# Kernel tuning notes

Hardware: AMD Instinct MI355X
Metric: run time of the kernel (lower is better)

Reference implementation:

```python
import jax, jax.numpy as jnp
import numpy as np

NUM_SEGMENTS = 16
N_MAX = 256
CHUNK = (N_MAX + NUM_SEGMENTS - 1) // NUM_SEGMENTS  # 16
BETA1, BETA2, BETA3 = 0.5, 0.5, 0.4


def _masked_mean(x, mask):
    m = mask.astype(x.dtype)
    s = m.sum()
    return jnp.where(s > 0, (x * m).sum() / jnp.maximum(s, 1.0), jnp.zeros((), x.dtype))


def setup_inputs() -> dict:
    key = jax.random.key(0)
    ks = jax.random.split(key, 10)
    B, S, H, V, Sm, R = 2, 1024, 4096, 32000, 256, 256
    k_hidden = jax.random.normal(ks[0], (B, S, H), dtype=jnp.float32)
    last_hidden = jax.random.normal(ks[1], (B, S, H), dtype=jnp.float32)
    input_ids = jax.random.randint(ks[2], (B, S), 0, V)
    attention_mask = jnp.ones((B, S), dtype=jnp.int32)
    starts = jax.random.randint(ks[3], (B,), 0, 300)
    ends = starts + 200 + jax.random.randint(ks[4], (B,), 0, 100)
    math_lengths = jnp.full((B,), Sm, dtype=jnp.int64 if jax.config.jax_enable_x64 else jnp.int32)
    math_labels = jax.random.randint(ks[5], (B, Sm), 0, V)
    math_attention_mask = jnp.ones((B, Sm), dtype=jnp.int32)
    A_matrices = jax.random.normal(ks[6], (NUM_SEGMENTS, H, R), dtype=jnp.float32) * 0.02
    B_matrices = jax.random.normal(ks[7], (NUM_SEGMENTS, R, H), dtype=jnp.float32) * 0.02
    bias = jnp.zeros((NUM_SEGMENTS, H), dtype=jnp.float32)
    W_lm = jax.random.normal(ks[8], (H, V), dtype=jnp.float32) * 0.02
    return {"k_hidden": k_hidden, "last_hidden": last_hidden, "input_ids": input_ids,
            "attention_mask": attention_mask, "starts": starts, "ends": ends,
            "math_lengths": math_lengths, "math_labels": math_labels,
            "math_attention_mask": math_attention_mask, "A_matrices": A_matrices,
            "B_matrices": B_matrices, "bias": bias, "W_lm": W_lm}


def reference(k_hidden, last_hidden, input_ids, attention_mask, starts, ends,
              math_lengths, math_labels, math_attention_mask,
              A_matrices, B_matrices, bias, W_lm):
    B, S, H = last_hidden.shape
    Sm = math_labels.shape[1]
    n_blk = Sm // CHUNK  # == NUM_SEGMENTS here (N_max == Sm)

    # ---- simple-talk / final-answer CE losses on full logits ----
    logits = jnp.einsum('bsh,hv->bsv', last_hidden, W_lm)  # [B,S,V]
    logp = jax.nn.log_softmax(logits[:, :-1, :], axis=-1)
    labels = input_ids[:, 1:]
    nll = -jnp.take_along_axis(logp, labels[..., None], axis=-1)[..., 0]  # [B,S-1]
    idx = jnp.arange(S - 1)[None, :]
    real_len = attention_mask.sum(axis=1)[:, None]
    mask_simple = (idx >= starts[:, None] - 1) & (idx <= ends[:, None] - 1)
    mask_final = (idx >= ends[:, None]) & (idx < real_len - 1)
    simple_talk_loss = _masked_mean(nll, mask_simple)
    final_answer_loss = _masked_mean(nll, mask_final)

    # ---- math loss: segment-routed LoRA (A @ (B @ h) + bias) then lm_head CE ----
    # mask_hidden selects the contiguous block [starts, starts+math_lengths) per row;
    # with full math_attention_mask this is exactly Sm tokens per row.
    pos = starts[:, None] + jnp.arange(Sm)[None, :]  # [B,Sm]
    math_h = jnp.take_along_axis(k_hidden, pos[:, :, None], axis=1)  # [B,Sm,H]
    # segment_ids are position//CHUNK -> contiguous blocks: grouped GEMM via reshape
    hb = math_h.reshape(B, n_blk, CHUNK, H)
    inter = jnp.einsum('bsch,srh->bscr', hb, B_matrices)      # B_seg @ h
    trans = jnp.einsum('bscr,shr->bsch', inter, A_matrices)   # A_seg @ inter
    trans = trans + bias[None, :, None, :]
    t = trans.reshape(B * Sm, H)
    mlogits = t @ W_lm                                        # [B*Sm, V]
    mlogp = jax.nn.log_softmax(mlogits, axis=-1)
    tgt = math_labels.reshape(-1)
    mnll = -jnp.take_along_axis(mlogp, tgt[:, None], axis=-1)[:, 0]  # [B*Sm]
    math_loss = mnll.mean()
    # per-segment mean losses (diagnostic, no-grad in original)
    A_losses = jax.lax.stop_gradient(mnll.reshape(B, n_blk, CHUNK).mean(axis=(0, 2)))

    total_loss = BETA1 * math_loss + BETA2 * simple_talk_loss + BETA3 * final_answer_loss
    return total_loss, math_loss, simple_talk_loss, final_answer_loss, A_losses
```

## Files before the change

### kernel.cpp

```cpp
#include <hip/hip_runtime.h>

#define NSEG 16
#define CH   16
#define Bb   2
#define Ss   1024
#define Hh   4096
#define Vv   32000
#define SMm  256
#define Rr   256

#define M_MAIN 2046
#define M_MATH 512
#define M_REAL 2558
#define M_PAD  2560

#define BM 128
#define BN 128
#define BK 128
#define NT_M (M_PAD/BM)
#define NT_N (Vv/BN)
#define KT   (Hh/BK)
#define NWG  (NT_M*NT_N)
#define NQG  (Hh/16)

#define HC   8
#define HCL  (Hh/HC)
#define PART_STRIDE (Bb*NSEG*CH*Rr)

typedef __attribute__((ext_vector_type(4))) float    floatx4;
typedef __attribute__((ext_vector_type(4))) int      intx4;
typedef __attribute__((ext_vector_type(8))) int      intx8;

#define ASCALE 16.f
#define WSCALE 256.f
#define DESCALE (1.f/(16.f*256.f))

template<bool W>
__device__ __forceinline__ int cvtpk(float a, float b, int old) {
  return __builtin_amdgcn_cvt_pk_fp8_f32(a, b, old, W);
}

__device__ __forceinline__ void gload_lds16(const void* g, void* l) {
  __builtin_amdgcn_global_load_lds((const __attribute__((address_space(1))) void*)g,
                                   (__attribute__((address_space(3))) void*)l, 16, 0, 0);
}

__global__ __launch_bounds__(256) void k_convA(const float* __restrict__ lh, intx4* __restrict__ Aq) {
  int row = blockIdx.x * 256 + threadIdx.x;
  int qgg = blockIdx.y;
  if (row >= M_MAIN) return;
  int b = row / (Ss - 1), s = row % (Ss - 1);
  const floatx4* src = (const floatx4*)(lh + ((size_t)(b * Ss + s)) * Hh + qgg * 16);
  floatx4 f0 = src[0], f1 = src[1], f2 = src[2], f3 = src[3];
  int p0 = cvtpk<false>(f0[0]*ASCALE, f0[1]*ASCALE, 0); p0 = cvtpk<true>(f0[2]*ASCALE, f0[3]*ASCALE, p0);
  int p1 = cvtpk<false>(f1[0]*ASCALE, f1[1]*ASCALE, 0); p1 = cvtpk<true>(f1[2]*ASCALE, f1[3]*ASCALE, p1);
  int p2 = cvtpk<false>(f2[0]*ASCALE, f2[1]*ASCALE, 0); p2 = cvtpk<true>(f2[2]*ASCALE, f2[3]*ASCALE, p2);
  int p3 = cvtpk<false>(f3[0]*ASCALE, f3[1]*ASCALE, 0); p3 = cvtpk<true>(f3[2]*ASCALE, f3[3]*ASCALE, p3);
  Aq[(size_t)qgg * M_PAD + row] = (intx4){p0, p1, p2, p3};
}

__global__ __launch_bounds__(256) void k_convW(const float* __restrict__ W, intx4* __restrict__ Wf) {
  int v = blockIdx.x * 256 + threadIdx.x;
  int qgg = blockIdx.y;
  const float* base = W + (size_t)(qgg * 16) * Vv + v;
  int p[4];
  #pragma unroll
  for (int q = 0; q < 4; ++q) {
    float e0 = base[(size_t)(4*q+0) * Vv] * WSCALE;
    float e1 = base[(size_t)(4*q+1) * Vv] * WSCALE;
    float e2 = base[(size_t)(4*q+2) * Vv] * WSCALE;
    float e3 = base[(size_t)(4*q+3) * Vv] * WSCALE;
    int pp = cvtpk<false>(e0, e1, 0);
    p[q] = cvtpk<true>(e2, e3, pp);
  }
  Wf[(size_t)qgg * Vv + v] = (intx4){p[0], p[1], p[2], p[3]};
}

__global__ __launch_bounds__(256) void k_inter2(const float* __restrict__ kh, const float* __restrict__ Bm,
                                                const int* __restrict__ starts, float* __restrict__ part) {
  int bid = blockIdx.x;
  int b = bid >> 7, seg = (bid >> 3) & 15, hc = bid & 7;
  int tid = threadIdx.x;
  __shared__ float sX[CH][HCL];
  int st = starts[b];
  for (int i = tid; i < CH * (HCL / 4); i += 256) {
    int c = i / (HCL / 4), k4 = i % (HCL / 4);
    int pos = st + seg * CH + c;
    ((floatx4*)&sX[c][0])[k4] = *(const floatx4*)(kh + ((size_t)(b * Ss + pos)) * Hh + hc * HCL + 4 * k4);
  }
  __syncthreads();
  const floatx4* w = (const floatx4*)(Bm + ((size_t)(seg * Rr + tid)) * Hh + hc * HCL);
  float acc[CH];
  #pragma unroll
  for (int c = 0; c < CH; ++c) acc[c] = 0.f;
  for (int i = 0; i < HCL / 4; ++i) {
    floatx4 w4 = w[i];
    #pragma unroll
    for (int c = 0; c < CH; ++c)
      acc[c] += w4[0]*sX[c][4*i] + w4[1]*sX[c][4*i+1] + w4[2]*sX[c][4*i+2] + w4[3]*sX[c][4*i+3];
  }
  float* dst = part + (size_t)hc * PART_STRIDE + ((size_t)(b * NSEG + seg)) * CH * Rr;
  #pragma unroll
  for (int c = 0; c < CH; ++c) dst[c * Rr + tid] = acc[c];
}

__global__ __launch_bounds__(256) void k_trans(const float* __restrict__ part, const float* __restrict__ Am,
                                               const float* __restrict__ bias, intx4* __restrict__ Aq) {
  int bid = blockIdx.x;
  int b = bid >> 7, seg = (bid >> 3) & 15, ht = bid & 7;
  int tid = threadIdx.x;
  __shared__ float sI[CH][Rr];
  const float* ib = part + ((size_t)(b * NSEG + seg)) * CH * Rr;
  for (int i = tid; i < CH * Rr / 4; i += 256) {
    floatx4 s = ((const floatx4*)ib)[i];
    #pragma unroll
    for (int hc = 1; hc < HC; ++hc)
      s += ((const floatx4*)(ib + (size_t)hc * PART_STRIDE))[i];
    ((floatx4*)&sI[0][0])[i] = s;
  }
  __syncthreads();
  unsigned char* Ab = (unsigned char*)Aq;
  for (int hh = 0; hh < 2; ++hh) {
    int h = (ht << 9) + (tid << 1) + hh;
    const floatx4* ar = (const floatx4*)(Am + ((size_t)(seg * Hh + h)) * Rr);
    float acc[CH];
    #pragma unroll
    for (int c = 0; c < CH; ++c) acc[c] = 0.f;
    for (int i = 0; i < Rr / 4; ++i) {
      floatx4 a4 = ar[i];
      #pragma unroll
      for (int c = 0; c < CH; ++c)
        acc[c] += a4[0]*sI[c][i*4] + a4[1]*sI[c][i*4+1] + a4[2]*sI[c][i*4+2] + a4[3]*sI[c][i*4+3];
    }
    float bv = bias[seg * Hh + h];
    #pragma unroll
    for (int c = 0; c < CH; ++c) {
      int row = M_MAIN + b * SMm + seg * CH + c;
      int pk = cvtpk<false>((acc[c] + bv) * ASCALE, 0.f, 0);
      Ab[(((size_t)(h >> 4)) * M_PAD + row) * 16 + (h & 15)] = (unsigned char)(pk & 0xFF);
    }
  }
}

__global__ __launch_bounds__(256) void k_labels(const int* __restrict__ input_ids, const int* __restrict__ mlab,
                                                int* __restrict__ labels, float* __restrict__ llog,
                                                intx4* __restrict__ Aq) {
  int t = blockIdx.x * 256 + threadIdx.x;
  if (t < M_PAD) {
    int lab;
    if (t < M_MAIN)      { int b = t / (Ss - 1), s = t % (Ss - 1); lab = input_ids[b * Ss + s + 1]; }
    else if (t < M_REAL) { lab = mlab[t - M_MAIN]; }
    else                 { lab = 0x7fffffff; }
    labels[t] = lab;
    llog[t] = 0.f;
  }
  if (t < 2 * NQG) {
    int qgg = t >> 1, row = M_REAL + (t & 1);
    Aq[(size_t)qgg * M_PAD + row] = (intx4){0, 0, 0, 0};
  }
}

__global__ __launch_bounds__(256, 4) void k_gemm_mx(const intx4* __restrict__ Aq, const intx4* __restrict__ Wf,
                                                    const int* __restrict__ labels, float* __restrict__ pmax,
                                                    float* __restrict__ psum, float* __restrict__ llog) {
  __shared__ intx4 As[BK/16][BM];
  __shared__ intx4 Bs[BK/16][BN];
  __shared__ float redM[BM * 2];
  __shared__ float redS[BM * 2];

  int bid = blockIdx.x;
  int mt = bid % NT_M, nt = bid / NT_M;
  int m0 = mt * BM, n0 = nt * BN;
  int tid = threadIdx.x;
  int lane = tid & 63, wid = tid >> 6;
  int wr = wid >> 1, wc = wid & 1;
  int l15 = lane & 15, l4 = lane >> 4;

  floatx4 acc[4][4];
  #pragma unroll
  for (int m = 0; m < 4; ++m)
    #pragma unroll
    for (int n = 0; n < 4; ++n) acc[m][n] = (floatx4){0.f, 0.f, 0.f, 0.f};

  for (int kt = 0; kt < KT; ++kt) {
    __syncthreads();
    #pragma unroll
    for (int it = 0; it < 4; ++it) {
      int ci = it * 256 + tid;
      int qg = ci >> 7, row = ci & 127;
      gload_lds16((const char*)Aq + (((size_t)(kt * 8 + qg) * M_PAD + m0 + row) << 4), &As[qg][row]);
    }
    #pragma unroll
    for (int it = 0; it < 4; ++it) {
      int ci = it * 256 + tid;
      int qg = ci >> 7, col = ci & 127;
      gload_lds16((const char*)Wf + (((size_t)(kt * 8 + qg) * Vv + n0 + col) << 4), &Bs[qg][col]);
    }
    __syncthreads();

    intx8 a[4], b[4];
    #pragma unroll
    for (int m = 0; m < 4; ++m) {
      int row = m * 16 + l15;
      intx4 lo = As[2 * l4][row];
      intx4 hi = As[2 * l4 + 1][row];
      a[m] = __builtin_shufflevector(lo, hi, 0, 1, 2, 3, 4, 5, 6, 7);
    }
    #pragma unroll
    for (int n = 0; n < 4; ++n) {
      int col = wc * 64 + n * 16 + l15;
      intx4 lo = Bs[2 * l4][col];
      intx4 hi = Bs[2 * l4 + 1][col];
      b[n] = __builtin_shufflevector(lo, hi, 0, 1, 2, 3, 4, 5, 6, 7);
    }
    #pragma unroll
    for (int m = 0; m < 4; ++m)
      #pragma unroll
      for (int n = 0; n < 4; ++n)
        acc[m][n] = __builtin_amdgcn_mfma_scale_f32_16x16x128_f8f6f4(
            a[m], b[n], acc[m][n], 0, 0, 0, 0x7F7F7F7F, 0, 0x7F7F7F7F);
  }

  #pragma unroll
  for (int m = 0; m < 4; ++m)
    #pragma unroll
    for (int n = 0; n < 4; ++n) acc[m][n] *= DESCALE;

  #pragma unroll
  for (int m = 0; m < 4; ++m) {
    #pragma unroll
    for (int r = 0; r < 4; ++r) {
      int grow = m0 + wr * 64 + m * 16 + l4 * 4 + r;
      int lab = (grow < M_REAL) ? labels[grow] : -1;
      #pragma unroll
      for (int n = 0; n < 4; ++n) {
        int gcol = n0 + wc * 64 + n * 16 + l15;
        if (lab == gcol) llog[grow] = acc[m][n][r];
      }
    }
  }
  float rm[4][4];
  #pragma unroll
  for (int m = 0; m < 4; ++m)
    #pragma unroll
    for (int r = 0; r < 4; ++r) {
      float v = fmaxf(fmaxf(acc[m][0][r], acc[m][1][r]), fmaxf(acc[m][2][r], acc[m][3][r]));
      v = fmaxf(v, __shfl_xor(v, 1));
      v = fmaxf(v, __shfl_xor(v, 2));
      v = fmaxf(v, __shfl_xor(v, 4));
      v = fmaxf(v, __shfl_xor(v, 8));
      rm[m][r] = v;
    }
  if (l15 == 0) {
    #pragma unroll
    for (int m = 0; m < 4; ++m)
      #pragma unroll
      for (int r = 0; r < 4; ++r)
        redM[(wr * 64 + m * 16 + l4 * 4 + r) * 2 + wc] = rm[m][r];
  }
  __syncthreads();
  #pragma unroll
  for (int m = 0; m < 4; ++m)
    #pragma unroll
    for (int r = 0; r < 4; ++r) {
      int row = wr * 64 + m * 16 + l4 * 4 + r;
      float tmx = fmaxf(redM[row * 2], redM[row * 2 + 1]);
      float s = 0.f;
      #pragma unroll
      for (int n = 0; n < 4; ++n) s += __expf(acc[m][n][r] - tmx);
      s += __shfl_xor(s, 1);
      s += __shfl_xor(s, 2);
      s += __shfl_xor(s, 4);
      s += __shfl_xor(s, 8);
      rm[m][r] = s;
    }
  if (l15 == 0) {
    #pragma unroll
    for (int m = 0; m < 4; ++m)
      #pragma unroll
      for (int r = 0; r < 4; ++r)
        redS[(wr * 64 + m * 16 + l4 * 4 + r) * 2 + wc] = rm[m][r];
  }
  __syncthreads();
  if (tid < BM) {
    int grow = m0 + tid;
    if (grow < M_REAL) {
      float tmx = fmaxf(redM[tid * 2], redM[tid * 2 + 1]);
      float s = redS[tid * 2] + redS[tid * 2 + 1];
      pmax[(size_t)grow * NT_N + nt] = tmx;
      psum[(size_t)grow * NT_N + nt] = s;
    }
  }
}

__global__ __launch_bounds__(256) void k_fin(const float* __restrict__ pmax, const float* __restrict__ psum,
                                             const float* __restrict__ llog, float* __restrict__ nll) {
  int row = blockIdx.x * 4 + (threadIdx.x >> 6);
  int lane = threadIdx.x & 63;
  if (row >= M_REAL) return;
  float m = -3.4e38f;
  for (int t = lane; t < NT_N; t += 64) m = fmaxf(m, pmax[(size_t)row * NT_N + t]);
  #pragma unroll
  for (int d = 1; d < 64; d <<= 1) m = fmaxf(m, __shfl_xor(m, d));
  float s = 0.f;
  for (int t = lane; t < NT_N; t += 64)
    s += psum[(size_t)row * NT_N + t] * __expf(pmax[(size_t)row * NT_N + t] - m);
  #pragma unroll
  for (int d = 1; d < 64; d <<= 1) s += __shfl_xor(s, d);
  if (lane == 0) nll[row] = logf(s) + m - llog[row];
}

__global__ __launch_bounds__(256) void k_loss(const float* __restrict__ nll, const int* __restrict__ starts,
                                              const int* __restrict__ ends, const int* __restrict__ attn,
                                              float* __restrict__ out) {
  __shared__ float rA[256], rB[256], rC[256], rD[256];
  __shared__ float smath[M_MATH];
  __shared__ float rl[2];
  int tid = threadIdx.x;
  for (int b = 0; b < 2; ++b) {
    float p = 0.f;
    for (int i = tid; i < Ss; i += 256) p += (float)attn[b * Ss + i];
    rA[tid] = p;
    __syncthreads();
    if (tid == 0) { float t = 0.f; for (int i = 0; i < 256; ++i) t += rA[i]; rl[b] = t; }
    __syncthreads();
  }
  float ss = 0.f, sc = 0.f, fs = 0.f, fc = 0.f;
  int st0 = starts[0], st1 = starts[1], en0 = ends[0], en1 = ends[1];
  for (int r = tid; r < M_MAIN; r += 256) {
    int b = r / (Ss - 1), idx = r % (Ss - 1);
    int st = b ? st1 : st0, en = b ? en1 : en0;
    int rlen = (int)rl[b];
    float v = nll[r];
    if (idx >= st - 1 && idx <= en - 1) { ss += v; sc += 1.f; }
    if (idx >= en && idx < rlen - 1)    { fs += v; fc += 1.f; }
  }
  rA[tid] = ss; rB[tid] = sc; rC[tid] = fs; rD[tid] = fc;
  for (int j = tid; j < M_MATH; j += 256) smath[j] = nll[M_MAIN + j];
  __syncthreads();
  if (tid == 0) {
    float SS = 0.f, SC = 0.f, FS = 0.f, FC = 0.f;
    for (int i = 0; i < 256; ++i) { SS += rA[i]; SC += rB[i]; FS += rC[i]; FC += rD[i]; }
    float MS = 0.f;
    for (int j = 0; j < M_MATH; ++j) MS += smath[j];
    float math_loss = MS / (float)M_MATH;
    float simple = (SC > 0.f) ? SS / fmaxf(SC, 1.f) : 0.f;
    float fin    = (FC > 0.f) ? FS / fmaxf(FC, 1.f) : 0.f;
    out[0] = 0.5f * math_loss + 0.5f * simple + 0.4f * fin;
    out[1] = math_loss;
    out[2] = simple;
    out[3] = fin;
    for (int seg = 0; seg < NSEG; ++seg) {
      float a = 0.f;
      for (int b = 0; b < 2; ++b)
        for (int c = 0; c < CH; ++c) a += smath[b * SMm + seg * CH + c];
      out[4 + seg] = a / 32.f;
    }
  }
}

extern "C" void kernel_launch(void* const* d_in, const int* in_sizes, int n_in,
                              void* d_out, int out_size, void* d_ws, size_t ws_size,
                              hipStream_t stream) {
  const float* k_hidden    = (const float*)d_in[0];
  const float* last_hidden = (const float*)d_in[1];
  const int*   input_ids   = (const int*)d_in[2];
  const int*   attn        = (const int*)d_in[3];
  const int*   starts      = (const int*)d_in[4];
  const int*   ends        = (const int*)d_in[5];
  const int*   math_labels = (const int*)d_in[7];
  const float* A_matrices  = (const float*)d_in[9];
  const float* B_matrices  = (const float*)d_in[10];
  const float* bias        = (const float*)d_in[11];
  const float* W_lm        = (const float*)d_in[12];
  float* out = (float*)d_out;

  char* ws = (char*)d_ws;
  size_t off = 0;
  intx4* Wf   = (intx4*)ws;                 off += (size_t)NQG * Vv * 16;
  intx4* Aq   = (intx4*)(ws + off);         off += (size_t)NQG * M_PAD * 16;
  float* part = (float*)(ws + off);         off += (size_t)HC * PART_STRIDE * 4;
  int*   labels = (int*)(ws + off);         off += (size_t)M_PAD * 4;
  float* llog   = (float*)(ws + off);       off += (size_t)M_PAD * 4;
  float* pmax   = (float*)(ws + off);       off += (size_t)M_PAD * NT_N * 4;
  float* psum   = (float*)(ws + off);       off += (size_t)M_PAD * NT_N * 4;
  float* nll    = (float*)(ws + off);       off += (size_t)M_PAD * 4;

  {
    dim3 ga((M_MAIN + 255) / 256, NQG);
    k_convA<<<ga, 256, 0, stream>>>(last_hidden, Aq);
  }
  k_inter2<<<Bb * NSEG * HC, 256, 0, stream>>>(k_hidden, B_matrices, starts, part);
  k_trans<<<Bb * NSEG * 8, 256, 0, stream>>>(part, A_matrices, bias, Aq);
  k_labels<<<(M_PAD + 255) / 256, 256, 0, stream>>>(input_ids, math_labels, labels, llog, Aq);
  {
    dim3 gw(Vv / 256, NQG);
    k_convW<<<gw, 256, 0, stream>>>(W_lm, Wf);
  }
  k_gemm_mx<<<NWG, 256, 0, stream>>>(Aq, Wf, labels, pmax, psum, llog);
  k_fin<<<(M_REAL + 3) / 4, 256, 0, stream>>>(pmax, psum, llog, nll);
  k_loss<<<1, 256, 0, stream>>>(nll, starts, ends, attn, out);
}
```

Before: 625.0 us.

## Enlarge GEMM tile to 256 rows and add triple-buffered async LDS pipeline

The FP8 MX GEMM now uses 512-thread workgroups with a 256x128 tile, so each W tile is reused across twice as many rows and the number of workgroups is halved. Global-to-LDS loads become a three-stage ring buffer issued two K-steps ahead, with vmcnt waits and a single barrier per iteration in place of the two syncthreads. Priority is raised around the MFMA block. This costs more LDS per block and lower occupancy, and the epilogue reduction must now handle the larger BM, which the hidden code may or may not do correctly.

```diff
diff --git a/kernel.cpp b/kernel.cpp
--- a/kernel.cpp
+++ b/kernel.cpp
@@ -14,7 +14,7 @@
 #define M_REAL 2558
 #define M_PAD  2560
 
-#define BM 128
+#define BM 256
 #define BN 128
 #define BK 128
 #define NT_M (M_PAD/BM)
@@ -160,11 +160,11 @@
   }
 }
 
-__global__ __launch_bounds__(256, 4) void k_gemm_mx(const intx4* __restrict__ Aq, const intx4* __restrict__ Wf,
-                                                    const int* __restrict__ labels, float* __restrict__ pmax,
-                                                    float* __restrict__ psum, float* __restrict__ llog) {
-  __shared__ intx4 As[BK/16][BM];
-  __shared__ intx4 Bs[BK/16][BN];
+__global__ __launch_bounds__(512, 2) void k_gemm_mx2(const intx4* __restrict__ Aq, const intx4* __restrict__ Wf,
+                                                     const int* __restrict__ labels, float* __restrict__ pmax,
+                                                     float* __restrict__ psum, float* __restrict__ llog) {
+  __shared__ intx4 As[3][8][BM];
+  __shared__ intx4 Bs[3][8][BN];
   __shared__ float redM[BM * 2];
   __shared__ float redS[BM * 2];
 
@@ -172,7 +172,8 @@
   int mt = bid % NT_M, nt = bid / NT_M;
   int m0 = mt * BM, n0 = nt * BN;
   int tid = threadIdx.x;
-  int lane = tid & 63, wid = tid >> 6;
+  int lane = tid & 63;
+  int wid = tid >> 6;
   int wr = wid >> 1, wc = wid & 1;
   int l15 = lane & 15, l4 = lane >> 4;
 
@@ -182,49 +183,73 @@
     #pragma unroll
     for (int n = 0; n < 4; ++n) acc[m][n] = (floatx4){0.f, 0.f, 0.f, 0.f};
 
+#define STAGE(tt, bb) do {                                                              \
+    const intx4* ab_ = Aq + (size_t)(tt) * 8 * M_PAD;                                   \
+    _Pragma("unroll")                                                                   \
+    for (int it_ = 0; it_ < 4; ++it_) {                                                 \
+      int s_ = it_ * 512 + tid;                                                         \
+      gload_lds16(ab_ + ((size_t)(s_ >> 8) * M_PAD + m0 + (s_ & 255)),                  \
+                  (void*)(&As[bb][0][0] + s_));                                         \
+    }                                                                                   \
+    const intx4* wb_ = Wf + (size_t)(tt) * 8 * Vv;                                      \
+    _Pragma("unroll")                                                                   \
+    for (int it_ = 0; it_ < 2; ++it_) {                                                 \
+      int s_ = it_ * 512 + tid;                                                         \
+      gload_lds16(wb_ + ((size_t)(s_ >> 7) * Vv + n0 + (s_ & 127)),                     \
+                  (void*)(&Bs[bb][0][0] + s_));                                         \
+    }                                                                                   \
+  } while (0)
+
+  STAGE(0, 0);
+  STAGE(1, 1);
+  int cur = 0;
+
   for (int kt = 0; kt < KT; ++kt) {
-    __syncthreads();
-    #pragma unroll
-    for (int it = 0; it < 4; ++it) {
-      int ci = it * 256 + tid;
-      int qg = ci >> 7, row = ci & 127;
-      gload_lds16((const char*)Aq + (((size_t)(kt * 8 + qg) * M_PAD + m0 + row) << 4), &As[qg][row]);
-    }
-    #pragma unroll
-    for (int it = 0; it < 4; ++it) {
-      int ci = it * 256 + tid;
-      int qg = ci >> 7, col = ci & 127;
-      gload_lds16((const char*)Wf + (((size_t)(kt * 8 + qg) * Vv + n0 + col) << 4), &Bs[qg][col]);
-    }
-    __syncthreads();
+    if (kt < KT - 1) {
+      asm volatile("s_waitcnt vmcnt(6)" ::: "memory");
+    } else {
+      asm volatile("s_waitcnt vmcnt(0)" ::: "memory");
+    }
+    __builtin_amdgcn_s_barrier();
+    __builtin_amdgcn_sched_barrier(0);
 
     intx8 a[4], b[4];
     #pragma unroll
     for (int m = 0; m < 4; ++m) {
-      int row = m * 16 + l15;
-      intx4 lo = As[2 * l4][row];
-      intx4 hi = As[2 * l4 + 1][row];
+      int row = wr * 64 + m * 16 + l15;
+      intx4 lo = As[cur][2 * l4][row];
+      intx4 hi = As[cur][2 * l4 + 1][row];
       a[m] = __builtin_shufflevector(lo, hi, 0, 1, 2, 3, 4, 5, 6, 7);
     }
     #pragma unroll
     for (int n = 0; n < 4; ++n) {
       int col = wc * 64 + n * 16 + l15;
-      intx4 lo = Bs[2 * l4][col];
-      intx4 hi = Bs[2 * l4 + 1][col];
+      intx4 lo = Bs[cur][2 * l4][col];
+      intx4 hi = Bs[cur][2 * l4 + 1][col];
       b[n] = __builtin_shufflevector(lo, hi, 0, 1, 2, 3, 4, 5, 6, 7);
     }
+
+    if (kt + 2 < KT) STAGE(kt + 2, (cur + 2) % 3);
+
+    __builtin_amdgcn_s_setprio(1);
     #pragma unroll
     for (int m = 0; m < 4; ++m)
       #pragma unroll
       for (int n = 0; n < 4; ++n)
         acc[m][n] = __builtin_amdgcn_mfma_scale_f32_16x16x128_f8f6f4(
             a[m], b[n], acc[m][n], 0, 0, 0, 0x7F7F7F7F, 0, 0x7F7F7F7F);
-  }
+    __builtin_amdgcn_s_setprio(0);
+
+    cur = (cur + 1) % 3;
+  }
+#undef STAGE
 
   #pragma unroll
   for (int m = 0; m < 4; ++m)
     #pragma unroll
     for (int n = 0; n < 4; ++n) acc[m][n] *= DESCALE;
+
+  __syncthreads();
 
   #pragma unroll
   for (int m = 0; m < 4; ++m) {
@@ -397,7 +422,7 @@
     dim3 gw(Vv / 256, NQG);
     k_convW<<<gw, 256, 0, stream>>>(W_lm, Wf);
   }
-  k_gemm_mx<<<NWG, 256, 0, stream>>>(Aq, Wf, labels, pmax, psum, llog);
+  k_gemm_mx2<<<NWG, 512, 0, stream>>>(Aq, Wf, labels, pmax, psum, llog);
   k_fin<<<(M_REAL + 3) / 4, 256, 0, stream>>>(pmax, psum, llog, nll);
   k_loss<<<1, 256, 0, stream>>>(nll, starts, ends, attn, out);
 }
```

Result: faster. 600.1 us (-4.0%).

## Double-buffer W tiles in LDS, load A directly to registers, swizzle blocks

Applied to the files above, without the earlier changes.

The FP8 MX GEMM main loop is restructured. The W tile for the next K step is now staged into a second LDS buffer while the current one is consumed, so each iteration needs only one barrier instead of two. The A operand skips LDS and is read per wave straight from global memory into registers. It also adds a block-index swizzle to group workgroups for L2 reuse, raises MFMA issue priority, and lowers the occupancy hint to 2 blocks per CU. The risks are extra global traffic for A, since rows are re-read by the two column waves, and higher register pressure.

```diff
diff --git a/kernel.cpp b/kernel.cpp
--- a/kernel.cpp
+++ b/kernel.cpp
@@ -21,6 +21,7 @@
 #define NT_N (Vv/BN)
 #define KT   (Hh/BK)
 #define NWG  (NT_M*NT_N)
+#define WPX  (NWG/8)
 #define NQG  (Hh/16)
 
 #define HC   8
@@ -160,19 +161,20 @@
   }
 }
 
-__global__ __launch_bounds__(256, 4) void k_gemm_mx(const intx4* __restrict__ Aq, const intx4* __restrict__ Wf,
+__global__ __launch_bounds__(256, 2) void k_gemm_hy(const intx4* __restrict__ Aq, const intx4* __restrict__ Wf,
                                                     const int* __restrict__ labels, float* __restrict__ pmax,
                                                     float* __restrict__ psum, float* __restrict__ llog) {
-  __shared__ intx4 As[BK/16][BM];
-  __shared__ intx4 Bs[BK/16][BN];
+  __shared__ intx4 Bs[2][8][BN];
   __shared__ float redM[BM * 2];
   __shared__ float redS[BM * 2];
 
   int bid = blockIdx.x;
-  int mt = bid % NT_M, nt = bid / NT_M;
+  int swz = (bid & 7) * WPX + (bid >> 3);
+  int mt = swz % NT_M, nt = swz / NT_M;
   int m0 = mt * BM, n0 = nt * BN;
   int tid = threadIdx.x;
-  int lane = tid & 63, wid = tid >> 6;
+  int lane = tid & 63;
+  int wid = tid >> 6;
   int wr = wid >> 1, wc = wid & 1;
   int l15 = lane & 15, l4 = lane >> 4;
 
@@ -182,49 +184,63 @@
     #pragma unroll
     for (int n = 0; n < 4; ++n) acc[m][n] = (floatx4){0.f, 0.f, 0.f, 0.f};
 
+  const intx4* pa = Aq + (size_t)(2 * l4) * M_PAD + m0 + wr * 64 + l15;
+
+#define STAGEB(bb, ktt) do {                                                   \
+    const intx4* wb_ = Wf + (size_t)((ktt) * 8) * Vv;                          \
+    _Pragma("unroll")                                                          \
+    for (int it_ = 0; it_ < 4; ++it_) {                                        \
+      int ci_ = it_ * 256 + tid;                                               \
+      gload_lds16(wb_ + (size_t)(ci_ >> 7) * Vv + n0 + (ci_ & 127),            \
+                  &Bs[bb][ci_ >> 7][ci_ & 127]);                               \
+    }                                                                          \
+  } while (0)
+
+  STAGEB(0, 0);
+
+  #pragma unroll 2
   for (int kt = 0; kt < KT; ++kt) {
+    int cb = kt & 1;
+    intx4 alo[4], ahi[4];
+    #pragma unroll
+    for (int m = 0; m < 4; ++m) {
+      alo[m] = pa[m * 16];
+      ahi[m] = pa[M_PAD + m * 16];
+    }
+    pa += 8 * (size_t)M_PAD;
+
     __syncthreads();
-    #pragma unroll
-    for (int it = 0; it < 4; ++it) {
-      int ci = it * 256 + tid;
-      int qg = ci >> 7, row = ci & 127;
-      gload_lds16((const char*)Aq + (((size_t)(kt * 8 + qg) * M_PAD + m0 + row) << 4), &As[qg][row]);
-    }
-    #pragma unroll
-    for (int it = 0; it < 4; ++it) {
-      int ci = it * 256 + tid;
-      int qg = ci >> 7, col = ci & 127;
-      gload_lds16((const char*)Wf + (((size_t)(kt * 8 + qg) * Vv + n0 + col) << 4), &Bs[qg][col]);
-    }
-    __syncthreads();
+    if (kt + 1 < KT) STAGEB(cb ^ 1, kt + 1);
 
     intx8 a[4], b[4];
     #pragma unroll
-    for (int m = 0; m < 4; ++m) {
-      int row = m * 16 + l15;
-      intx4 lo = As[2 * l4][row];
-      intx4 hi = As[2 * l4 + 1][row];
-      a[m] = __builtin_shufflevector(lo, hi, 0, 1, 2, 3, 4, 5, 6, 7);
-    }
+    for (int m = 0; m < 4; ++m)
+      a[m] = __builtin_shufflevector(alo[m], ahi[m], 0, 1, 2, 3, 4, 5, 6, 7);
     #pragma unroll
     for (int n = 0; n < 4; ++n) {
       int col = wc * 64 + n * 16 + l15;
-      intx4 lo = Bs[2 * l4][col];
-      intx4 hi = Bs[2 * l4 + 1][col];
+      intx4 lo = Bs[cb][2 * l4][col];
+      intx4 hi = Bs[cb][2 * l4 + 1][col];
       b[n] = __builtin_shufflevector(lo, hi, 0, 1, 2, 3, 4, 5, 6, 7);
     }
+
+    __builtin_amdgcn_s_setprio(1);
     #pragma unroll
     for (int m = 0; m < 4; ++m)
       #pragma unroll
       for (int n = 0; n < 4; ++n)
         acc[m][n] = __builtin_amdgcn_mfma_scale_f32_16x16x128_f8f6f4(
             a[m], b[n], acc[m][n], 0, 0, 0, 0x7F7F7F7F, 0, 0x7F7F7F7F);
-  }
+    __builtin_amdgcn_s_setprio(0);
+  }
+#undef STAGEB
 
   #pragma unroll
   for (int m = 0; m < 4; ++m)
     #pragma unroll
     for (int n = 0; n < 4; ++n) acc[m][n] *= DESCALE;
+
+  __syncthreads();
 
   #pragma unroll
   for (int m = 0; m < 4; ++m) {
@@ -397,7 +413,7 @@
     dim3 gw(Vv / 256, NQG);
     k_convW<<<gw, 256, 0, stream>>>(W_lm, Wf);
   }
-  k_gemm_mx<<<NWG, 256, 0, stream>>>(Aq, Wf, labels, pmax, psum, llog);
+  k_gemm_hy<<<NWG, 256, 0, stream>>>(Aq, Wf, labels, pmax, psum, llog);
   k_fin<<<(M_REAL + 3) / 4, 256, 0, stream>>>(pmax, psum, llog, nll);
   k_loss<<<1, 256, 0, stream>>>(nll, starts, ends, attn, out);
 }
```

After: 686.5 us. 9.8% more time.
